# Optimization experiments

Measured on AMD Instinct MI355X. Metric: run time of the kernel, lower is better.

## Reference

```python
import jax, jax.numpy as jnp
import numpy as np


def setup_inputs() -> dict:
    key = jax.random.key(0)
    ks = jax.random.split(key, 4)
    B, S, D, F, E = 2, 2048, 1024, 2048, 8
    x = jax.random.normal(ks[0], (B, S, D), dtype=jnp.float32)
    router_w = jax.random.normal(ks[1], (D, E), dtype=jnp.float32) * 0.02
    w_in = jax.random.normal(ks[2], (E, D, 2 * F), dtype=jnp.float32) * 0.02
    w_out = jax.random.normal(ks[3], (E, F, D), dtype=jnp.float32) * 0.02
    out_bias = jnp.zeros((D,), dtype=jnp.float32)
    return {"x": x, "router_w": router_w, "w_in": w_in, "w_out": w_out,
            "out_bias": out_bias, "top_k": 2}


def reference(x, router_w, w_in, w_out, out_bias, top_k):
    B, S, D = x.shape
    E = router_w.shape[1]
    xt = x.reshape(-1, D)                      # [T, D]
    T = xt.shape[0]

    # --- top-k router (JetMoeTopKGating) ---
    logits = xt @ router_w                     # [T, E]
    top_vals, top_idx = jax.lax.top_k(logits, top_k)   # [T, k]
    gates = jax.nn.softmax(top_vals, axis=-1)          # [T, k], softmax over selected
    # dense combine weights [T, E]: gate where selected, 0 elsewhere
    combine = jnp.zeros((T, E), dtype=x.dtype).at[
        jnp.arange(T)[:, None], top_idx].add(gates)

    # --- grouped expert MLP (GLU: silu(h1) * h2) ---
    out = jnp.zeros((T, D), dtype=x.dtype)
    for e in range(E):                         # E is small & static
        h = xt @ w_in[e]                       # [T, 2F]
        g, v = jnp.split(h, 2, axis=-1)
        y = (jax.nn.silu(g) * v) @ w_out[e]    # [T, D]
        out = out + combine[:, e:e + 1] * y
    out = out.reshape(B, S, D) + out_bias

    # --- load-balancing aux loss ---
    probs = jax.nn.softmax(logits, axis=-1)    # [T, E]
    # fraction of routed assignments per expert
    sel = jax.nn.one_hot(top_idx, E, dtype=x.dtype).sum(axis=1)  # [T, E]
    f = sel.mean(axis=0) / top_k               # [E]
    P = probs.mean(axis=0)                     # [E]
    aux_loss = E * jnp.sum(f * P)
    return out, aux_loss
```

## Files before the change

kernel.cpp:

```cpp
#include <hip/hip_runtime.h>


#define T_TOK 4096
#define DIM   1024
#define NEXP  8
#define FF    2048
#define YB    24

typedef __attribute__((ext_vector_type(8))) short short8;
typedef __attribute__((ext_vector_type(4))) float f32x4;

__device__ __forceinline__ unsigned short f2b(float f) {
  unsigned int u = __builtin_bit_cast(unsigned int, f);
  u += 0x7fffu + ((u >> 16) & 1u);
  return (unsigned short)(u >> 16);
}

__device__ __forceinline__ void gll16(const unsigned short* g, unsigned short* l) {
  __builtin_amdgcn_global_load_lds(
      (const __attribute__((address_space(1))) unsigned int*)g,
      (__attribute__((address_space(3))) unsigned int*)l, 16, 0, 0);
}

__global__ void router_k(const float* __restrict__ x, const float* __restrict__ rw,
                         int* __restrict__ tok_e, float* __restrict__ tok_g,
                         float* __restrict__ psum_part) {
  const int t = blockIdx.x * 4 + (threadIdx.x >> 6);
  const int lane = threadIdx.x & 63;
  double acc[8];
#pragma unroll
  for (int e = 0; e < 8; e++) acc[e] = 0.0;
  const float* xr = x + (size_t)t * DIM;
  for (int d = lane; d < DIM; d += 64) {
    double xv = (double)xr[d];
#pragma unroll
    for (int e = 0; e < 8; e++) acc[e] += xv * (double)rw[d * 8 + e];
  }
#pragma unroll
  for (int off = 32; off > 0; off >>= 1) {
#pragma unroll
    for (int e = 0; e < 8; e++) acc[e] += __shfl_down(acc[e], off, 64);
  }
  __shared__ float pblk[8];
  if (threadIdx.x < 8) pblk[threadIdx.x] = 0.f;
  __syncthreads();
  if (lane == 0) {
    int i0 = -1, i1 = -1;
    double v0 = -1e300, v1 = -1e300;
#pragma unroll
    for (int e = 0; e < 8; e++) {
      double v = acc[e];
      if (v > v0) { v1 = v0; i1 = i0; v0 = v; i0 = e; }
      else if (v > v1) { v1 = v; i1 = e; }
    }
    float g1 = 1.f / (1.f + __expf((float)(v0 - v1)));
    tok_e[t * 2] = i0; tok_e[t * 2 + 1] = i1;
    tok_g[t * 2] = 1.f - g1; tok_g[t * 2 + 1] = g1;
    float s = 0.f; float p[8];
#pragma unroll
    for (int e = 0; e < 8; e++) { p[e] = __expf((float)(acc[e] - v0)); s += p[e]; }
    float inv = 1.f / s;
#pragma unroll
    for (int e = 0; e < 8; e++) atomicAdd(&pblk[e], p[e] * inv);
  }
  __syncthreads();
  if (threadIdx.x < 8) psum_part[blockIdx.x * 8 + threadIdx.x] = pblk[threadIdx.x];
}

__global__ __launch_bounds__(1024) void bucket_k(
    const int* __restrict__ tok_e, const float* __restrict__ tok_g,
    const float* __restrict__ psum_part,
    int* __restrict__ cnt, int* __restrict__ off,
    int* __restrict__ slot_t, float* __restrict__ slot_g,
    float* __restrict__ out_aux) {
  const int tid = threadIdx.x;
  const int lane = tid & 63;
  __shared__ int lcnt[8];
  __shared__ float fsum[8];
  if (tid < 8) { lcnt[tid] = 0; fsum[tid] = 0.f; }
  __syncthreads();
#pragma unroll
  for (int rep = 0; rep < 4; rep++) {
    const int t = rep * 1024 + tid;
    const int e0 = tok_e[t * 2], e1 = tok_e[t * 2 + 1];
    const float g0 = tok_g[t * 2], g1 = tok_g[t * 2 + 1];
#pragma unroll
    for (int which = 0; which < 2; which++) {
      const int e = which ? e1 : e0;
      const float g = which ? g1 : g0;
      int slot = 0;
#pragma unroll
      for (int ex = 0; ex < 8; ex++) {
        unsigned long long m = __ballot(e == ex);
        int base = 0;
        int first = __ffsll((long long)m) - 1;
        if (m != 0ull && lane == first) base = atomicAdd(&lcnt[ex], __popcll(m));
        base = __shfl(base, first & 63, 64);
        if (e == ex) slot = base + __popcll(m & ((1ull << lane) - 1ull));
      }
      slot_t[e * T_TOK + slot] = t;
      slot_g[e * T_TOK + slot] = g;
    }
  }
  float p[8];
#pragma unroll
  for (int e = 0; e < 8; e++) p[e] = psum_part[tid * 8 + e];
#pragma unroll
  for (int o = 32; o > 0; o >>= 1) {
#pragma unroll
    for (int e = 0; e < 8; e++) p[e] += __shfl_down(p[e], o, 64);
  }
  if (lane == 0) {
#pragma unroll
    for (int e = 0; e < 8; e++) atomicAdd(&fsum[e], p[e]);
  }
  __syncthreads();
  if (tid == 0) {
    int o = 0; float aux = 0.f;
    for (int e = 0; e < 8; e++) {
      cnt[e] = lcnt[e]; off[e] = o; o += lcnt[e];
      aux += ((float)lcnt[e] / (4096.f * 2.f)) * (fsum[e] / 4096.f);
    }
    out_aux[0] = 8.f * aux;
  }
}

__global__ void init_out_k(float* __restrict__ out, const float* __restrict__ bias) {
  int i = blockIdx.x * 256 + threadIdx.x;
  out[i] = bias[i & (DIM - 1)];
}

__global__ void transpose_k(const float* __restrict__ src, unsigned short* __restrict__ dst,
                            int K, int N) {
  __shared__ float tile[64][65];
  const int e = blockIdx.z;
  const int kb = blockIdx.y * 64, nb = blockIdx.x * 64;
  const float* s = src + (size_t)e * K * N;
  unsigned short* d = dst + (size_t)e * N * K;
  const int tid = threadIdx.x;
  const int r = tid >> 2;
  const int cseg = (tid & 3) * 16;
#pragma unroll
  for (int j = 0; j < 16; j += 4) {
    float4 v = *(const float4*)(s + (size_t)(kb + r) * N + nb + cseg + j);
    tile[r][cseg + j] = v.x; tile[r][cseg + j + 1] = v.y;
    tile[r][cseg + j + 2] = v.z; tile[r][cseg + j + 3] = v.w;
  }
  __syncthreads();
#pragma unroll
  for (int j = 0; j < 16; j += 4) {
    ushort4 o4;
    o4.x = f2b(tile[cseg + j][r]);
    o4.y = f2b(tile[cseg + j + 1][r]);
    o4.z = f2b(tile[cseg + j + 2][r]);
    o4.w = f2b(tile[cseg + j + 3][r]);
    *(ushort4*)(d + (size_t)(nb + r) * K + kb + cseg + j) = o4;
  }
}

__global__ void gather_k(const float* __restrict__ x, const int* __restrict__ cnt,
                         const int* __restrict__ off, const int* __restrict__ slot_t,
                         unsigned short* __restrict__ A1) {
  const int e = blockIdx.z;
  const int rb = blockIdx.y * 128;
  const int c = cnt[e];
  if (rb >= c) return;
  const int o = off[e];
  for (int i = threadIdx.x; i < 128 * 256; i += 256) {
    int r = i >> 8;
    int seg = (i & 255) * 4;
    int row = rb + r;
    if (row >= c) continue;
    int t = slot_t[e * T_TOK + row];
    float4 v = *(const float4*)(x + (size_t)t * DIM + seg);
    ushort4 o4;
    o4.x = f2b(v.x); o4.y = f2b(v.y); o4.z = f2b(v.z); o4.w = f2b(v.w);
    *(ushort4*)(A1 + (size_t)(o + row) * DIM + seg) = o4;
  }
}

__global__ __launch_bounds__(256, 2) void gemm1_k(
    const unsigned short* __restrict__ A1, const unsigned short* __restrict__ W1T,
    unsigned short* __restrict__ H, const int* __restrict__ cnt, const int* __restrict__ off) {
  const int e = blockIdx.z;
  const int c = cnt[e];
  const int rb = blockIdx.y * 128;
  if (rb >= c) return;
  const int o = off[e];
  const unsigned short* Ab = A1 + (size_t)(o + rb) * DIM;
  const unsigned short* Bgb = W1T + ((size_t)e * 4096 + blockIdx.x * 128) * DIM;
  const unsigned short* Bvb = Bgb + (size_t)2048 * DIM;

  __shared__ __align__(16) unsigned short As[128][32];
  __shared__ __align__(16) unsigned short Bg[128][32];
  __shared__ __align__(16) unsigned short Bv[128][32];

  const int tid = threadIdx.x;
  const int lane = tid & 63;
  const int w = tid >> 6;
  const int mq = (w >> 1) * 64;
  const int nq = (w & 1) * 64;
  const int fr = lane & 15;
  const int fq = (lane >> 4) * 8;

  const int s0 = w * 128 + lane;
  const int r0 = s0 >> 2, c0 = (s0 & 3) * 8;
  const int s1 = s0 + 64;
  const int r1 = s1 >> 2, c1 = (s1 & 3) * 8;

  f32x4 accg[4][4], accv[4][4];
  const f32x4 zero = {0.f, 0.f, 0.f, 0.f};
#pragma unroll
  for (int i = 0; i < 4; i++)
#pragma unroll
    for (int j = 0; j < 4; j++) { accg[i][j] = zero; accv[i][j] = zero; }

  for (int k0 = 0; k0 < DIM; k0 += 32) {
    gll16(Ab  + (size_t)r0 * DIM + k0 + c0, &As[r0][c0]);
    gll16(Ab  + (size_t)r1 * DIM + k0 + c1, &As[r1][c1]);
    gll16(Bgb + (size_t)r0 * DIM + k0 + c0, &Bg[r0][c0]);
    gll16(Bgb + (size_t)r1 * DIM + k0 + c1, &Bg[r1][c1]);
    gll16(Bvb + (size_t)r0 * DIM + k0 + c0, &Bv[r0][c0]);
    gll16(Bvb + (size_t)r1 * DIM + k0 + c1, &Bv[r1][c1]);
    __syncthreads();

    short8 af[4], bgf[4], bvf[4];
#pragma unroll
    for (int mi = 0; mi < 4; mi++)
      af[mi] = __builtin_bit_cast(short8, *(const uint4*)&As[mq + mi * 16 + fr][fq]);
#pragma unroll
    for (int ni = 0; ni < 4; ni++) {
      bgf[ni] = __builtin_bit_cast(short8, *(const uint4*)&Bg[nq + ni * 16 + fr][fq]);
      bvf[ni] = __builtin_bit_cast(short8, *(const uint4*)&Bv[nq + ni * 16 + fr][fq]);
    }
#pragma unroll
    for (int mi = 0; mi < 4; mi++)
#pragma unroll
      for (int ni = 0; ni < 4; ni++) {
        accg[mi][ni] = __builtin_amdgcn_mfma_f32_16x16x32_bf16(af[mi], bgf[ni], accg[mi][ni], 0, 0, 0);
        accv[mi][ni] = __builtin_amdgcn_mfma_f32_16x16x32_bf16(af[mi], bvf[ni], accv[mi][ni], 0, 0, 0);
      }
    __syncthreads();
  }

  const int vrows = c - rb;
  const int cb = blockIdx.x * 128;
#pragma unroll
  for (int mi = 0; mi < 4; mi++) {
#pragma unroll
    for (int ni = 0; ni < 4; ni++) {
      const int col = nq + ni * 16 + fr;
      const int rowb = mq + mi * 16 + (lane >> 4) * 4;
#pragma unroll
      for (int r = 0; r < 4; r++) {
        const int row = rowb + r;
        if (row < vrows) {
          float g = accg[mi][ni][r];
          float v = accv[mi][ni][r];
          float s = g / (1.f + __expf(-g)) * v;
          H[(size_t)(o + rb + row) * FF + cb + col] = f2b(s);
        }
      }
    }
  }
}

__global__ __launch_bounds__(256, 2) void gemm2_k(
    const unsigned short* __restrict__ H, const unsigned short* __restrict__ W2T,
    float* __restrict__ out, const int* __restrict__ cnt, const int* __restrict__ off,
    const int* __restrict__ slot_t, const float* __restrict__ slot_g) {
  const int e = blockIdx.z;
  const int c = cnt[e];
  const int rb = blockIdx.y * 128;
  if (rb >= c) return;
  const int o = off[e];
  const unsigned short* Ab = H + (size_t)(o + rb) * FF;
  const unsigned short* Bb = W2T + ((size_t)e * 1024 + blockIdx.x * 128) * FF;

  __shared__ __align__(16) unsigned short As[128][32];
  __shared__ __align__(16) unsigned short Bs[128][32];

  const int tid = threadIdx.x;
  const int lane = tid & 63;
  const int w = tid >> 6;
  const int mq = (w >> 1) * 64;
  const int nq = (w & 1) * 64;
  const int fr = lane & 15;
  const int fq = (lane >> 4) * 8;

  const int s0 = w * 128 + lane;
  const int r0 = s0 >> 2, c0 = (s0 & 3) * 8;
  const int s1 = s0 + 64;
  const int r1 = s1 >> 2, c1 = (s1 & 3) * 8;

  f32x4 acc[4][4];
  const f32x4 zero = {0.f, 0.f, 0.f, 0.f};
#pragma unroll
  for (int i = 0; i < 4; i++)
#pragma unroll
    for (int j = 0; j < 4; j++) acc[i][j] = zero;

  for (int k0 = 0; k0 < FF; k0 += 32) {
    gll16(Ab + (size_t)r0 * FF + k0 + c0, &As[r0][c0]);
    gll16(Ab + (size_t)r1 * FF + k0 + c1, &As[r1][c1]);
    gll16(Bb + (size_t)r0 * FF + k0 + c0, &Bs[r0][c0]);
    gll16(Bb + (size_t)r1 * FF + k0 + c1, &Bs[r1][c1]);
    __syncthreads();

    short8 af[4], bf[4];
#pragma unroll
    for (int mi = 0; mi < 4; mi++)
      af[mi] = __builtin_bit_cast(short8, *(const uint4*)&As[mq + mi * 16 + fr][fq]);
#pragma unroll
    for (int ni = 0; ni < 4; ni++)
      bf[ni] = __builtin_bit_cast(short8, *(const uint4*)&Bs[nq + ni * 16 + fr][fq]);
#pragma unroll
    for (int mi = 0; mi < 4; mi++)
#pragma unroll
      for (int ni = 0; ni < 4; ni++)
        acc[mi][ni] = __builtin_amdgcn_mfma_f32_16x16x32_bf16(af[mi], bf[ni], acc[mi][ni], 0, 0, 0);
    __syncthreads();
  }

  const int vrows = c - rb;
  const int cb = blockIdx.x * 128;
#pragma unroll
  for (int mi = 0; mi < 4; mi++) {
    const int rowb = mq + mi * 16 + (lane >> 4) * 4;
#pragma unroll
    for (int r = 0; r < 4; r++) {
      const int row = rowb + r;
      if (row < vrows) {
        const int t = slot_t[e * T_TOK + rb + row];
        const float gt = slot_g[e * T_TOK + rb + row];
        float* orow = out + (size_t)t * DIM + cb;
#pragma unroll
        for (int ni = 0; ni < 4; ni++) {
          const int col = nq + ni * 16 + fr;
          atomicAdd(orow + col, gt * acc[mi][ni][r]);
        }
      }
    }
  }
}

extern "C" void kernel_launch(void* const* d_in, const int* in_sizes, int n_in,
                              void* d_out, int out_size, void* d_ws, size_t ws_size,
                              hipStream_t stream) {
  const float* x     = (const float*)d_in[0];
  const float* rw    = (const float*)d_in[1];
  const float* w_in  = (const float*)d_in[2];
  const float* w_out = (const float*)d_in[3];
  const float* bias  = (const float*)d_in[4];
  float* out = (float*)d_out;

  char* ws = (char*)d_ws;
  int*   cnt    = (int*)ws;
  int*   off    = (int*)(ws + 32);
  int*   slot_t = (int*)(ws + 256);
  float* slot_g = (float*)(ws + 256 + 131072);
  int*   tok_e  = (int*)(ws + (512 << 10));
  float* tok_g  = (float*)(ws + (576 << 10));
  float* psum_p = (float*)(ws + (640 << 10));
  unsigned short* A1  = (unsigned short*)(ws + ((size_t)1 << 20));
  unsigned short* H   = (unsigned short*)(ws + ((size_t)18 << 20));
  unsigned short* W1T = (unsigned short*)(ws + ((size_t)51 << 20));
  unsigned short* W2T = (unsigned short*)(ws + ((size_t)116 << 20));

  init_out_k<<<16384, 256, 0, stream>>>(out, bias);
  transpose_k<<<dim3(64, 16, 8), 256, 0, stream>>>(w_in, W1T, 1024, 4096);
  transpose_k<<<dim3(16, 32, 8), 256, 0, stream>>>(w_out, W2T, 2048, 1024);
  router_k<<<1024, 256, 0, stream>>>(x, rw, tok_e, tok_g, psum_p);
  bucket_k<<<1, 1024, 0, stream>>>(tok_e, tok_g, psum_p, cnt, off,
                                   slot_t, slot_g, out + (size_t)T_TOK * DIM);
  gather_k<<<dim3(1, YB, 8), 256, 0, stream>>>(x, cnt, off, slot_t, A1);
  gemm1_k<<<dim3(16, YB, 8), 256, 0, stream>>>(A1, W1T, H, cnt, off);
  gemm2_k<<<dim3(8, YB, 8), 256, 0, stream>>>(H, W2T, out, cnt, off, slot_t, slot_g);
}
```

Before: 572.6 us.

## Double GEMM K-tile to 64 with XOR-swizzled LDS, parallelize gather and vectorize router

Both expert GEMMs now stage 64-wide K tiles instead of 32, using a rotated (swizzled) LDS layout so fragment reads avoid bank conflicts. This halves the number of barrier pairs per K loop and makes each global load more coalesced. The gather kernel is split across 8 column blocks for more parallelism, and the router loads x as float4. LDS use per block doubles (48KB in gemm1), which may limit occupancy.

```diff
diff --git a/kernel.cpp b/kernel.cpp
--- a/kernel.cpp
+++ b/kernel.cpp
@@ -6,6 +6,7 @@
 #define NEXP  8
 #define FF    2048
 #define YB    24
+#define BK    64
 
 typedef __attribute__((ext_vector_type(8))) short short8;
 typedef __attribute__((ext_vector_type(4))) float f32x4;
@@ -20,6 +21,26 @@
   __builtin_amdgcn_global_load_lds(
       (const __attribute__((address_space(1))) unsigned int*)g,
       (__attribute__((address_space(3))) unsigned int*)l, 16, 0, 0);
+}
+
+__device__ __forceinline__ void stage_tile(const unsigned short* __restrict__ gbase,
+                                           size_t ldk, int k0,
+                                           unsigned short* __restrict__ lds,
+                                           int w, int lane) {
+#pragma unroll
+  for (int i = 0; i < 4; i++) {
+    const int s = w * 256 + i * 64 + lane;
+    const int r = s >> 3;
+    const int pc = s & 7;
+    const int gc = ((pc - r) & 7) * 8;
+    gll16(gbase + (size_t)r * ldk + k0 + gc, lds + (size_t)s * 8);
+  }
+}
+
+__device__ __forceinline__ short8 frag_read(const unsigned short* __restrict__ lds,
+                                            int row, int kk, int quad) {
+  const int p = ((kk * 4 + quad) + row) & 7;
+  return __builtin_bit_cast(short8, *(const uint4*)(lds + (size_t)row * BK + p * 8));
 }
 
 __global__ void router_k(const float* __restrict__ x, const float* __restrict__ rw,
@@ -31,10 +52,17 @@
 #pragma unroll
   for (int e = 0; e < 8; e++) acc[e] = 0.0;
   const float* xr = x + (size_t)t * DIM;
-  for (int d = lane; d < DIM; d += 64) {
-    double xv = (double)xr[d];
-#pragma unroll
-    for (int e = 0; e < 8; e++) acc[e] += xv * (double)rw[d * 8 + e];
+#pragma unroll
+  for (int d0 = 0; d0 < DIM; d0 += 256) {
+    const int d = d0 + lane * 4;
+    float4 xv = *(const float4*)(xr + d);
+    const float* rwr = rw + d * 8;
+#pragma unroll
+    for (int j = 0; j < 4; j++) {
+      double xd = (double)((j == 0) ? xv.x : (j == 1) ? xv.y : (j == 2) ? xv.z : xv.w);
+#pragma unroll
+      for (int e = 0; e < 8; e++) acc[e] += xd * (double)rwr[j * 8 + e];
+    }
   }
 #pragma unroll
   for (int off = 32; off > 0; off >>= 1) {
@@ -166,9 +194,10 @@
   const int c = cnt[e];
   if (rb >= c) return;
   const int o = off[e];
-  for (int i = threadIdx.x; i < 128 * 256; i += 256) {
-    int r = i >> 8;
-    int seg = (i & 255) * 4;
+  const int cb = blockIdx.x * 128;
+  for (int i = threadIdx.x; i < 128 * 32; i += 256) {
+    int r = i >> 5;
+    int seg = cb + (i & 31) * 4;
     int row = rb + r;
     if (row >= c) continue;
     int t = slot_t[e * T_TOK + row];
@@ -191,9 +220,9 @@
   const unsigned short* Bgb = W1T + ((size_t)e * 4096 + blockIdx.x * 128) * DIM;
   const unsigned short* Bvb = Bgb + (size_t)2048 * DIM;
 
-  __shared__ __align__(16) unsigned short As[128][32];
-  __shared__ __align__(16) unsigned short Bg[128][32];
-  __shared__ __align__(16) unsigned short Bv[128][32];
+  __shared__ __align__(16) unsigned short As[128][BK];
+  __shared__ __align__(16) unsigned short Bg[128][BK];
+  __shared__ __align__(16) unsigned short Bv[128][BK];
 
   const int tid = threadIdx.x;
   const int lane = tid & 63;
@@ -201,12 +230,7 @@
   const int mq = (w >> 1) * 64;
   const int nq = (w & 1) * 64;
   const int fr = lane & 15;
-  const int fq = (lane >> 4) * 8;
-
-  const int s0 = w * 128 + lane;
-  const int r0 = s0 >> 2, c0 = (s0 & 3) * 8;
-  const int s1 = s0 + 64;
-  const int r1 = s1 >> 2, c1 = (s1 & 3) * 8;
+  const int quad = lane >> 4;
 
   f32x4 accg[4][4], accv[4][4];
   const f32x4 zero = {0.f, 0.f, 0.f, 0.f};
@@ -215,31 +239,31 @@
 #pragma unroll
     for (int j = 0; j < 4; j++) { accg[i][j] = zero; accv[i][j] = zero; }
 
-  for (int k0 = 0; k0 < DIM; k0 += 32) {
-    gll16(Ab  + (size_t)r0 * DIM + k0 + c0, &As[r0][c0]);
-    gll16(Ab  + (size_t)r1 * DIM + k0 + c1, &As[r1][c1]);
-    gll16(Bgb + (size_t)r0 * DIM + k0 + c0, &Bg[r0][c0]);
-    gll16(Bgb + (size_t)r1 * DIM + k0 + c1, &Bg[r1][c1]);
-    gll16(Bvb + (size_t)r0 * DIM + k0 + c0, &Bv[r0][c0]);
-    gll16(Bvb + (size_t)r1 * DIM + k0 + c1, &Bv[r1][c1]);
+  for (int k0 = 0; k0 < DIM; k0 += BK) {
+    stage_tile(Ab,  DIM, k0, &As[0][0], w, lane);
+    stage_tile(Bgb, DIM, k0, &Bg[0][0], w, lane);
+    stage_tile(Bvb, DIM, k0, &Bv[0][0], w, lane);
     __syncthreads();
 
-    short8 af[4], bgf[4], bvf[4];
-#pragma unroll
-    for (int mi = 0; mi < 4; mi++)
-      af[mi] = __builtin_bit_cast(short8, *(const uint4*)&As[mq + mi * 16 + fr][fq]);
-#pragma unroll
-    for (int ni = 0; ni < 4; ni++) {
-      bgf[ni] = __builtin_bit_cast(short8, *(const uint4*)&Bg[nq + ni * 16 + fr][fq]);
-      bvf[ni] = __builtin_bit_cast(short8, *(const uint4*)&Bv[nq + ni * 16 + fr][fq]);
-    }
-#pragma unroll
-    for (int mi = 0; mi < 4; mi++)
+#pragma unroll
+    for (int kk = 0; kk < 2; kk++) {
+      short8 af[4], bgf[4], bvf[4];
+#pragma unroll
+      for (int mi = 0; mi < 4; mi++)
+        af[mi] = frag_read(&As[0][0], mq + mi * 16 + fr, kk, quad);
 #pragma unroll
       for (int ni = 0; ni < 4; ni++) {
-        accg[mi][ni] = __builtin_amdgcn_mfma_f32_16x16x32_bf16(af[mi], bgf[ni], accg[mi][ni], 0, 0, 0);
-        accv[mi][ni] = __builtin_amdgcn_mfma_f32_16x16x32_bf16(af[mi], bvf[ni], accv[mi][ni], 0, 0, 0);
+        bgf[ni] = frag_read(&Bg[0][0], nq + ni * 16 + fr, kk, quad);
+        bvf[ni] = frag_read(&Bv[0][0], nq + ni * 16 + fr, kk, quad);
       }
+#pragma unroll
+      for (int mi = 0; mi < 4; mi++)
+#pragma unroll
+        for (int ni = 0; ni < 4; ni++) {
+          accg[mi][ni] = __builtin_amdgcn_mfma_f32_16x16x32_bf16(af[mi], bgf[ni], accg[mi][ni], 0, 0, 0);
+          accv[mi][ni] = __builtin_amdgcn_mfma_f32_16x16x32_bf16(af[mi], bvf[ni], accv[mi][ni], 0, 0, 0);
+        }
+    }
     __syncthreads();
   }
 
@@ -250,7 +274,7 @@
 #pragma unroll
     for (int ni = 0; ni < 4; ni++) {
       const int col = nq + ni * 16 + fr;
-      const int rowb = mq + mi * 16 + (lane >> 4) * 4;
+      const int rowb = mq + mi * 16 + quad * 4;
 #pragma unroll
       for (int r = 0; r < 4; r++) {
         const int row = rowb + r;
@@ -277,8 +301,8 @@
   const unsigned short* Ab = H + (size_t)(o + rb) * FF;
   const unsigned short* Bb = W2T + ((size_t)e * 1024 + blockIdx.x * 128) * FF;
 
-  __shared__ __align__(16) unsigned short As[128][32];
-  __shared__ __align__(16) unsigned short Bs[128][32];
+  __shared__ __align__(16) unsigned short As[128][BK];
+  __shared__ __align__(16) unsigned short Bs[128][BK];
 
   const int tid = threadIdx.x;
   const int lane = tid & 63;
@@ -286,12 +310,7 @@
   const int mq = (w >> 1) * 64;
   const int nq = (w & 1) * 64;
   const int fr = lane & 15;
-  const int fq = (lane >> 4) * 8;
-
-  const int s0 = w * 128 + lane;
-  const int r0 = s0 >> 2, c0 = (s0 & 3) * 8;
-  const int s1 = s0 + 64;
-  const int r1 = s1 >> 2, c1 = (s1 & 3) * 8;
+  const int quad = lane >> 4;
 
   f32x4 acc[4][4];
   const f32x4 zero = {0.f, 0.f, 0.f, 0.f};
@@ -300,25 +319,26 @@
 #pragma unroll
     for (int j = 0; j < 4; j++) acc[i][j] = zero;
 
-  for (int k0 = 0; k0 < FF; k0 += 32) {
-    gll16(Ab + (size_t)r0 * FF + k0 + c0, &As[r0][c0]);
-    gll16(Ab + (size_t)r1 * FF + k0 + c1, &As[r1][c1]);
-    gll16(Bb + (size_t)r0 * FF + k0 + c0, &Bs[r0][c0]);
-    gll16(Bb + (size_t)r1 * FF + k0 + c1, &Bs[r1][c1]);
+  for (int k0 = 0; k0 < FF; k0 += BK) {
+    stage_tile(Ab, FF, k0, &As[0][0], w, lane);
+    stage_tile(Bb, FF, k0, &Bs[0][0], w, lane);
     __syncthreads();
 
-    short8 af[4], bf[4];
-#pragma unroll
-    for (int mi = 0; mi < 4; mi++)
-      af[mi] = __builtin_bit_cast(short8, *(const uint4*)&As[mq + mi * 16 + fr][fq]);
-#pragma unroll
-    for (int ni = 0; ni < 4; ni++)
-      bf[ni] = __builtin_bit_cast(short8, *(const uint4*)&Bs[nq + ni * 16 + fr][fq]);
-#pragma unroll
-    for (int mi = 0; mi < 4; mi++)
+#pragma unroll
+    for (int kk = 0; kk < 2; kk++) {
+      short8 af[4], bf[4];
+#pragma unroll
+      for (int mi = 0; mi < 4; mi++)
+        af[mi] = frag_read(&As[0][0], mq + mi * 16 + fr, kk, quad);
 #pragma unroll
       for (int ni = 0; ni < 4; ni++)
-        acc[mi][ni] = __builtin_amdgcn_mfma_f32_16x16x32_bf16(af[mi], bf[ni], acc[mi][ni], 0, 0, 0);
+        bf[ni] = frag_read(&Bs[0][0], nq + ni * 16 + fr, kk, quad);
+#pragma unroll
+      for (int mi = 0; mi < 4; mi++)
+#pragma unroll
+        for (int ni = 0; ni < 4; ni++)
+          acc[mi][ni] = __builtin_amdgcn_mfma_f32_16x16x32_bf16(af[mi], bf[ni], acc[mi][ni], 0, 0, 0);
+    }
     __syncthreads();
   }
 
@@ -326,7 +346,7 @@
   const int cb = blockIdx.x * 128;
 #pragma unroll
   for (int mi = 0; mi < 4; mi++) {
-    const int rowb = mq + mi * 16 + (lane >> 4) * 4;
+    const int rowb = mq + mi * 16 + quad * 4;
 #pragma unroll
     for (int r = 0; r < 4; r++) {
       const int row = rowb + r;
@@ -373,7 +393,7 @@
   router_k<<<1024, 256, 0, stream>>>(x, rw, tok_e, tok_g, psum_p);
   bucket_k<<<1, 1024, 0, stream>>>(tok_e, tok_g, psum_p, cnt, off,
                                    slot_t, slot_g, out + (size_t)T_TOK * DIM);
-  gather_k<<<dim3(1, YB, 8), 256, 0, stream>>>(x, cnt, off, slot_t, A1);
+  gather_k<<<dim3(8, YB, 8), 256, 0, stream>>>(x, cnt, off, slot_t, A1);
   gemm1_k<<<dim3(16, YB, 8), 256, 0, stream>>>(A1, W1T, H, cnt, off);
   gemm2_k<<<dim3(8, YB, 8), 256, 0, stream>>>(H, W2T, out, cnt, off, slot_t, slot_g);
 }
```

After: 481.3 us. 1.19x faster.
